# Kernel tuning notes

Hardware: AMD Instinct MI355X
Metric: run time of the kernel (lower is better)

The kernel has to match this reference:

```python
import jax, jax.numpy as jnp
import numpy as np

O = 128      # o_size
E = 512      # embed_dim
H = 128      # h_size
V = 34       # num_letter
B = 2048     # batch
T = 512      # listener timesteps
EPS = 1e-5   # BatchNorm eps


def _lstm_cell(x, h, c, W_ih, W_hh, b_ih, b_hh):
    # PyTorch LSTMCell: gates ordered i, f, g, o
    g = x @ W_ih.T + b_ih + h @ W_hh.T + b_hh
    i, f, gg, o = jnp.split(g, 4, axis=1)
    c_new = jax.nn.sigmoid(f) * c + jax.nn.sigmoid(i) * jnp.tanh(gg)
    h_new = jax.nn.sigmoid(o) * jnp.tanh(c_new)
    return h_new, c_new


def setup_inputs() -> dict:
    key = jax.random.key(0)
    ks = jax.random.split(key, 32)
    d = {}
    d['hk'] = jax.random.normal(ks[0], (B, T, O), jnp.float32)
    d['hv'] = jax.random.normal(ks[1], (B, T, O), jnp.float32)
    d['y_1'] = jax.random.normal(ks[2], (B, E), jnp.float32)
    d['c_1'] = jax.random.normal(ks[3], (B, O), jnp.float32)
    d['sh_1'] = jax.random.normal(ks[4], (3, B, O), jnp.float32)
    d['sc_1'] = jax.random.normal(ks[5], (3, B, O), jnp.float32)
    d['mask'] = jnp.ones((B, T), jnp.float32)
    s = 0.05
    in_dims = [O + E, O, O]
    for l in range(3):
        d[f'W_ih{l}'] = jax.random.normal(ks[6 + 4 * l], (4 * O, in_dims[l]), jnp.float32) * s
        d[f'W_hh{l}'] = jax.random.normal(ks[7 + 4 * l], (4 * O, O), jnp.float32) * s
        d[f'b_ih{l}'] = jax.random.normal(ks[8 + 4 * l], (4 * O,), jnp.float32) * s
        d[f'b_hh{l}'] = jax.random.normal(ks[9 + 4 * l], (4 * O,), jnp.float32) * s
    d['w1'] = jax.random.normal(ks[20], (H, O), jnp.float32) * s
    d['b1'] = jnp.zeros((H,), jnp.float32)
    d['w2'] = jax.random.normal(ks[21], (H, O), jnp.float32) * s
    d['b2'] = jnp.zeros((H,), jnp.float32)
    d['w3'] = jax.random.normal(ks[22], (V, H), jnp.float32) * s
    d['b3'] = jnp.zeros((V,), jnp.float32)
    d['gamma'] = jnp.ones((H,), jnp.float32)
    d['beta'] = jnp.zeros((H,), jnp.float32)
    return d


def reference(hk, hv, y_1, c_1, sh_1, sc_1, mask,
              W_ih0, W_hh0, b_ih0, b_hh0,
              W_ih1, W_hh1, b_ih1, b_hh1,
              W_ih2, W_hh2, b_ih2, b_hh2,
              w1, b1, w2, b2, w3, b3, gamma, beta):
    x0 = jnp.concatenate((y_1, c_1), axis=1)            # [B, E+O]
    sh0, sc0 = _lstm_cell(x0, sh_1[0], sc_1[0], W_ih0, W_hh0, b_ih0, b_hh0)
    sh1, sc1 = _lstm_cell(sh0, sh_1[1], sc_1[1], W_ih1, W_hh1, b_ih1, b_hh1)
    sh2, sc2 = _lstm_cell(sh1, sh_1[2], sc_1[2], W_ih2, W_hh2, b_ih2, b_hh2)

    # Attention: query is the CELL state sc2 (as in the original code)
    scores = jnp.einsum('bto,bo->bt', hk, sc2)           # [B, T]
    p = jax.nn.softmax(scores, axis=1)
    p = p * mask
    p = p / jnp.sum(p, axis=1, keepdims=True)            # mask-then-renormalize
    c = jnp.einsum('bt,bto->bo', p, hv)                  # [B, O]

    out = sh2 @ w1.T + b1 + (c @ w2.T + b2)              # [B, H]
    # BatchNorm1d (training mode: batch statistics, biased variance)
    mu = jnp.mean(out, axis=0)
    var = jnp.mean((out - mu) ** 2, axis=0)
    out = gamma * (out - mu) * jax.lax.rsqrt(var + EPS) + beta
    out = jax.nn.relu(out)
    out = out @ w3.T + b3                                # [B, V]
    out = jax.nn.softmax(out, axis=1)
    return out, c, jnp.stack([sh0, sh1, sh2]), jnp.stack([sc0, sc1, sc2])
```

## Files before the change

### kernel.cpp

```cpp
#include <hip/hip_runtime.h>
#include <hip/hip_bf16.h>

#define BSZ 2048
#define TSZ 512
#define OSZ 128
#define ESZ 512
#define HSZ 128
#define VSZ 34

#define OFF_C   69632
#define OFF_SH  331776
#define OFF_SC  1118208
#define LAYER   262144

typedef __attribute__((ext_vector_type(8))) short s16x8;
typedef __attribute__((ext_vector_type(4))) float f32x4;

__device__ __forceinline__ float sigf(float x)  { return 1.0f / (1.0f + __expf(-x)); }
__device__ __forceinline__ float tanhf_(float x){ return 2.0f / (1.0f + __expf(-2.0f * x)) - 1.0f; }

__device__ __forceinline__ short f2b(float f) {
    return (short)__bfloat16_as_ushort(__float2bfloat16(f));
}

struct F8 { float4 lo, hi; };

__global__ __launch_bounds__(256) void lstm_cell_mfma(
    const float* __restrict__ A0, int w0,
    const float* __restrict__ A1, int w1,
    const float* __restrict__ A2,
    const float* __restrict__ Wih, int in_dim,
    const float* __restrict__ Whh,
    const float* __restrict__ bih, const float* __restrict__ bhh,
    const float* __restrict__ c_prev,
    float* __restrict__ h_out, float* __restrict__ c_out,
    int K)
{
    __shared__ short lsA[64 * 32];
    __shared__ short lsB[64 * 32];

    const int tid = threadIdx.x;
    const int bm = blockIdx.x * 64;
    const int j0 = blockIdx.y * 16;

    const int sRow = tid >> 2;
    const int sKc  = (tid & 3) << 3;
    const int sOff = sRow * 32 + ((((tid & 3)) ^ (sRow & 3)) << 3);

    const int w_row = (sRow >> 4) * 128 + j0 + (sRow & 15);

    const int wav = tid >> 6, lan = tid & 63;
    const int fr  = lan & 15;
    const int fkb = lan >> 4;
    const int aOff = (wav * 16 + fr) * 32 + ((fkb ^ (fr & 3)) << 3);
    const int bOffBase = fr * 32 + ((fkb ^ (fr & 3)) << 3);

    const int j = j0 + fr;

    f32x4 acc[4];
#pragma unroll
    for (int t = 0; t < 4; ++t) {
        float bv = bih[t * 128 + j] + bhh[t * 128 + j];
        acc[t] = (f32x4){bv, bv, bv, bv};
    }

    auto loadA = [&](int kt) -> F8 {
        int kg = kt * 32 + sKc;
        const float* p;
        if (kg < w0)           p = A0 + (size_t)(bm + sRow) * w0 + kg;
        else if (kg < w0 + w1) p = A1 + (size_t)(bm + sRow) * w1 + (kg - w0);
        else                   p = A2 + (size_t)(bm + sRow) * 128 + (kg - w0 - w1);
        F8 r; r.lo = *(const float4*)p; r.hi = *(const float4*)(p + 4); return r;
    };
    auto loadB = [&](int kt) -> F8 {
        int kg = kt * 32 + sKc;
        const float* p;
        if (kg < in_dim) p = Wih + (size_t)w_row * in_dim + kg;
        else             p = Whh + (size_t)w_row * 128 + (kg - in_dim);
        F8 r; r.lo = *(const float4*)p; r.hi = *(const float4*)(p + 4); return r;
    };

    const int nk = K >> 5;
    F8 aV = loadA(0);
    F8 bV = loadB(0);

    for (int kt = 0; kt < nk; ++kt) {
        s16x8 ap, bp;
        ap[0] = f2b(aV.lo.x); ap[1] = f2b(aV.lo.y); ap[2] = f2b(aV.lo.z); ap[3] = f2b(aV.lo.w);
        ap[4] = f2b(aV.hi.x); ap[5] = f2b(aV.hi.y); ap[6] = f2b(aV.hi.z); ap[7] = f2b(aV.hi.w);
        bp[0] = f2b(bV.lo.x); bp[1] = f2b(bV.lo.y); bp[2] = f2b(bV.lo.z); bp[3] = f2b(bV.lo.w);
        bp[4] = f2b(bV.hi.x); bp[5] = f2b(bV.hi.y); bp[6] = f2b(bV.hi.z); bp[7] = f2b(bV.hi.w);
        *(s16x8*)(lsA + sOff) = ap;
        *(s16x8*)(lsB + sOff) = bp;
        __syncthreads();
        if (kt + 1 < nk) { aV = loadA(kt + 1); bV = loadB(kt + 1); }

        s16x8 af = *(const s16x8*)(lsA + aOff);
#pragma unroll
        for (int t = 0; t < 4; ++t) {
            s16x8 bf = *(const s16x8*)(lsB + bOffBase + t * 512);
            acc[t] = __builtin_amdgcn_mfma_f32_16x16x32_bf16(af, bf, acc[t], 0, 0, 0);
        }
        __syncthreads();
    }

#pragma unroll
    for (int r = 0; r < 4; ++r) {
        int row = bm + wav * 16 + fkb * 4 + r;
        float gi = acc[0][r], gf = acc[1][r], gg = acc[2][r], go = acc[3][r];
        float cp = c_prev[(size_t)row * 128 + j];
        float cn = sigf(gf) * cp + sigf(gi) * tanhf_(gg);
        float hn = sigf(go) * tanhf_(cn);
        c_out[(size_t)row * 128 + j] = cn;
        h_out[(size_t)row * 128 + j] = hn;
    }
}

__global__ __launch_bounds__(256) void attn_kernel(
    const float* __restrict__ hk, const float* __restrict__ hv,
    const float* __restrict__ mask, const float* __restrict__ sc2,
    float* __restrict__ c_out)
{
    const int b = blockIdx.x;
    const int tid = threadIdx.x;
    __shared__ float sP[512];
    __shared__ float sRed[8];
    __shared__ float sC[8][128];

    const float* hkb = hk + (size_t)b * (TSZ * OSZ);
    const int og = (tid & 31) * 4;
    const int tg = tid >> 5;
    float4 q = *(const float4*)(sc2 + (size_t)b * 128 + og);

    for (int it = 0; it < 64; ++it) {
        float4 v = *(const float4*)(hkb + it * 1024 + tid * 4);
        float d = v.x * q.x + v.y * q.y + v.z * q.z + v.w * q.w;
        d += __shfl_xor(d, 1, 32);
        d += __shfl_xor(d, 2, 32);
        d += __shfl_xor(d, 4, 32);
        d += __shfl_xor(d, 8, 32);
        d += __shfl_xor(d, 16, 32);
        if ((tid & 31) == 0) sP[it * 8 + tg] = d;
    }
    __syncthreads();

    float m = fmaxf(sP[tid], sP[tid + 256]);
#pragma unroll
    for (int off = 1; off < 64; off <<= 1) m = fmaxf(m, __shfl_xor(m, off, 64));
    if ((tid & 63) == 0) sRed[tid >> 6] = m;
    __syncthreads();
    m = fmaxf(fmaxf(sRed[0], sRed[1]), fmaxf(sRed[2], sRed[3]));

    const float* mk = mask + (size_t)b * TSZ;
    float e0 = __expf(sP[tid] - m) * mk[tid];
    float e1 = __expf(sP[tid + 256] - m) * mk[tid + 256];
    float s = e0 + e1;
#pragma unroll
    for (int off = 1; off < 64; off <<= 1) s += __shfl_xor(s, off, 64);
    if ((tid & 63) == 0) sRed[4 + (tid >> 6)] = s;
    __syncthreads();
    float inv = 1.0f / (sRed[4] + sRed[5] + sRed[6] + sRed[7]);
    sP[tid]       = e0 * inv;
    sP[tid + 256] = e1 * inv;
    __syncthreads();

    float4 acc = {0.f, 0.f, 0.f, 0.f};
    const float* hvb = hv + (size_t)b * (TSZ * OSZ);
    for (int it = 0; it < 64; ++it) {
        float p = sP[it * 8 + tg];
        float4 v = *(const float4*)(hvb + it * 1024 + tid * 4);
        acc.x += p * v.x; acc.y += p * v.y; acc.z += p * v.z; acc.w += p * v.w;
    }
    *(float4*)&sC[tg][og] = acc;
    __syncthreads();
    if (tid < 128) {
        float r = 0.f;
#pragma unroll
        for (int g = 0; g < 8; ++g) r += sC[g][tid];
        c_out[(size_t)b * 128 + tid] = r;
    }
}

__global__ __launch_bounds__(256) void head_pre_kernel(
    const float* __restrict__ sh2, const float* __restrict__ cvec,
    const float* __restrict__ w1, const float* __restrict__ b1,
    const float* __restrict__ w2, const float* __restrict__ b2,
    float* __restrict__ out_pre, float* __restrict__ sum_part,
    float* __restrict__ sq_part)
{
    __shared__ float xs[8][128];
    __shared__ float xc[8][128];
    __shared__ float ps[2][128];
    __shared__ float pq[2][128];
    const int tid = threadIdx.x;
    const int rb = blockIdx.x * 8;
    {
        int row = tid >> 5, off = (tid & 31) * 4;
        *(float4*)&xs[row][off] = *(const float4*)(sh2 + (size_t)(rb + row) * 128 + off);
        *(float4*)&xc[row][off] = *(const float4*)(cvec + (size_t)(rb + row) * 128 + off);
    }
    __syncthreads();

    const int col = tid & 127, rg = tid >> 7;
    float acc[4];
    float bb = b1[col] + b2[col];
#pragma unroll
    for (int r = 0; r < 4; ++r) acc[r] = bb;
    const float* w1r = w1 + (size_t)col * 128;
    const float* w2r = w2 + (size_t)col * 128;
    for (int k4 = 0; k4 < 32; ++k4) {
        float4 wa = *(const float4*)(w1r + k4 * 4);
        float4 wb = *(const float4*)(w2r + k4 * 4);
#pragma unroll
        for (int r = 0; r < 4; ++r) {
            float4 xa = *(const float4*)&xs[rg * 4 + r][k4 * 4];
            float4 xb = *(const float4*)&xc[rg * 4 + r][k4 * 4];
            acc[r] += xa.x * wa.x + xa.y * wa.y + xa.z * wa.z + xa.w * wa.w
                    + xb.x * wb.x + xb.y * wb.y + xb.z * wb.z + xb.w * wb.w;
        }
    }
    float s = 0.f, q = 0.f;
#pragma unroll
    for (int r = 0; r < 4; ++r) {
        out_pre[(size_t)(rb + rg * 4 + r) * 128 + col] = acc[r];
        s += acc[r]; q += acc[r] * acc[r];
    }
    ps[rg][col] = s; pq[rg][col] = q;
    __syncthreads();
    if (rg == 0) {
        sum_part[blockIdx.x * 128 + col] = ps[0][col] + ps[1][col];
        sq_part[blockIdx.x * 128 + col]  = pq[0][col] + pq[1][col];
    }
}

__global__ __launch_bounds__(256) void bn_stats_kernel(
    const float* __restrict__ sum_part, const float* __restrict__ sq_part,
    float* __restrict__ mu_out, float* __restrict__ rstd_out)
{
    __shared__ float s2[2][128], q2[2][128];
    const int tid = threadIdx.x;
    const int col = tid & 127, h = tid >> 7;
    float s = 0.f, q = 0.f;
    for (int p = h * 128; p < h * 128 + 128; ++p) {
        s += sum_part[p * 128 + col];
        q += sq_part[p * 128 + col];
    }
    s2[h][col] = s; q2[h][col] = q;
    __syncthreads();
    if (h == 0) {
        float st = s2[0][col] + s2[1][col];
        float qt = q2[0][col] + q2[1][col];
        float mu = st * (1.0f / 2048.0f);
        float var = qt * (1.0f / 2048.0f) - mu * mu;
        mu_out[col] = mu;
        rstd_out[col] = rsqrtf(var + 1e-5f);
    }
}

__global__ __launch_bounds__(256) void head_post_kernel(
    const float* __restrict__ out_pre, const float* __restrict__ mu_buf,
    const float* __restrict__ rstd_buf, const float* __restrict__ gamma,
    const float* __restrict__ beta, const float* __restrict__ w3,
    const float* __restrict__ b3, float* __restrict__ out0)
{
    __shared__ float xn[8][128];
    __shared__ float lg[8][34];
    const int tid = threadIdx.x;
    const int rb = blockIdx.x * 8;
    {
        int row = tid >> 5, off = (tid & 31) * 4;
        float4 v   = *(const float4*)(out_pre + (size_t)(rb + row) * 128 + off);
        float4 mu4 = *(const float4*)(mu_buf + off);
        float4 rs4 = *(const float4*)(rstd_buf + off);
        float4 g4  = *(const float4*)(gamma + off);
        float4 b4  = *(const float4*)(beta + off);
        float4 o;
        o.x = fmaxf(g4.x * (v.x - mu4.x) * rs4.x + b4.x, 0.0f);
        o.y = fmaxf(g4.y * (v.y - mu4.y) * rs4.y + b4.y, 0.0f);
        o.z = fmaxf(g4.z * (v.z - mu4.z) * rs4.z + b4.z, 0.0f);
        o.w = fmaxf(g4.w * (v.w - mu4.w) * rs4.w + b4.w, 0.0f);
        *(float4*)&xn[row][off] = o;
    }
    __syncthreads();

    for (int idx = tid; idx < 8 * VSZ; idx += 256) {
        int row = idx / VSZ, vv = idx % VSZ;
        const float* w3r = w3 + (size_t)vv * 128;
        float acc = b3[vv];
        for (int k4 = 0; k4 < 32; ++k4) {
            float4 x4 = *(const float4*)&xn[row][k4 * 4];
            float4 wv = *(const float4*)(w3r + k4 * 4);
            acc += x4.x * wv.x + x4.y * wv.y + x4.z * wv.z + x4.w * wv.w;
        }
        lg[row][vv] = acc;
    }
    __syncthreads();

    const int row = tid >> 5, lane = tid & 31;
    float m = -1e30f;
    for (int vv = lane; vv < VSZ; vv += 32) m = fmaxf(m, lg[row][vv]);
#pragma unroll
    for (int off = 1; off < 32; off <<= 1) m = fmaxf(m, __shfl_xor(m, off, 32));
    float e0 = __expf(lg[row][lane] - m);
    float e1 = (lane + 32 < VSZ) ? __expf(lg[row][lane + 32] - m) : 0.0f;
    float s = e0 + e1;
#pragma unroll
    for (int off = 1; off < 32; off <<= 1) s += __shfl_xor(s, off, 32);
    float inv = 1.0f / s;
    out0[(size_t)(rb + row) * VSZ + lane] = e0 * inv;
    if (lane + 32 < VSZ) out0[(size_t)(rb + row) * VSZ + lane + 32] = e1 * inv;
}

extern "C" void kernel_launch(void* const* d_in, const int* in_sizes, int n_in,
                              void* d_out, int out_size, void* d_ws, size_t ws_size,
                              hipStream_t stream)
{
    const float* hk   = (const float*)d_in[0];
    const float* hv   = (const float*)d_in[1];
    const float* y_1  = (const float*)d_in[2];
    const float* c_1  = (const float*)d_in[3];
    const float* sh_1 = (const float*)d_in[4];
    const float* sc_1 = (const float*)d_in[5];
    const float* mask = (const float*)d_in[6];
    const float* Wih0 = (const float*)d_in[7];
    const float* Whh0 = (const float*)d_in[8];
    const float* bih0 = (const float*)d_in[9];
    const float* bhh0 = (const float*)d_in[10];
    const float* Wih1 = (const float*)d_in[11];
    const float* Whh1 = (const float*)d_in[12];
    const float* bih1 = (const float*)d_in[13];
    const float* bhh1 = (const float*)d_in[14];
    const float* Wih2 = (const float*)d_in[15];
    const float* Whh2 = (const float*)d_in[16];
    const float* bih2 = (const float*)d_in[17];
    const float* bhh2 = (const float*)d_in[18];
    const float* w1   = (const float*)d_in[19];
    const float* b1   = (const float*)d_in[20];
    const float* w2   = (const float*)d_in[21];
    const float* b2   = (const float*)d_in[22];
    const float* w3   = (const float*)d_in[23];
    const float* b3   = (const float*)d_in[24];
    const float* gamma= (const float*)d_in[25];
    const float* beta = (const float*)d_in[26];

    float* out   = (float*)d_out;
    float* outC  = out + OFF_C;
    float* outSH = out + OFF_SH;
    float* outSC = out + OFF_SC;

    float* ws       = (float*)d_ws;
    float* out_pre  = ws;
    float* sum_part = ws + 262144;
    float* sq_part  = sum_part + 32768;
    float* mu_buf   = sq_part + 32768;
    float* rstd_buf = mu_buf + 128;

    dim3 gG(32, 8), bG(256);
    lstm_cell_mfma<<<gG, bG, 0, stream>>>(
        y_1, 512, c_1, 128, sh_1, Wih0, 640, Whh0, bih0, bhh0,
        sc_1, outSH, outSC, 768);
    lstm_cell_mfma<<<gG, bG, 0, stream>>>(
        outSH, 128, nullptr, 0, sh_1 + LAYER, Wih1, 128, Whh1, bih1, bhh1,
        sc_1 + LAYER, outSH + LAYER, outSC + LAYER, 256);
    lstm_cell_mfma<<<gG, bG, 0, stream>>>(
        outSH + LAYER, 128, nullptr, 0, sh_1 + 2 * LAYER, Wih2, 128, Whh2, bih2, bhh2,
        sc_1 + 2 * LAYER, outSH + 2 * LAYER, outSC + 2 * LAYER, 256);
    attn_kernel<<<BSZ, 256, 0, stream>>>(hk, hv, mask, outSC + 2 * LAYER, outC);
    head_pre_kernel<<<256, 256, 0, stream>>>(outSH + 2 * LAYER, outC, w1, b1, w2, b2,
                                             out_pre, sum_part, sq_part);
    bn_stats_kernel<<<1, 256, 0, stream>>>(sum_part, sq_part, mu_buf, rstd_buf);
    head_post_kernel<<<256, 256, 0, stream>>>(out_pre, mu_buf, rstd_buf, gamma, beta,
                                              w3, b3, out);
}
```

Baseline: 277.7 us.

## Stage hk through swizzled LDS with register prefetch in attention scores

The score phase now loads 8 timesteps' worth of hk into registers, writes them to a swizzled 32KB shared-memory tile, and prefetches the next chunk while computing dot products. Each thread handles a quarter of a row, so only two shuffles are needed instead of five. The hv loop is also unrolled by 8. The goal is more memory-level parallelism and less shuffle overhead, at the cost of extra LDS use, which may lower occupancy, and extra syncs.

```diff
diff --git a/kernel.cpp b/kernel.cpp
--- a/kernel.cpp
+++ b/kernel.cpp
@@ -123,26 +123,53 @@
 {
     const int b = blockIdx.x;
     const int tid = threadIdx.x;
+    __shared__ float sK[64 * 128];
     __shared__ float sP[512];
     __shared__ float sRed[8];
     __shared__ float sC[8][128];
 
     const float* hkb = hk + (size_t)b * (TSZ * OSZ);
-    const int og = (tid & 31) * 4;
-    const int tg = tid >> 5;
-    float4 q = *(const float4*)(sc2 + (size_t)b * 128 + og);
-
-    for (int it = 0; it < 64; ++it) {
-        float4 v = *(const float4*)(hkb + it * 1024 + tid * 4);
-        float d = v.x * q.x + v.y * q.y + v.z * q.z + v.w * q.w;
-        d += __shfl_xor(d, 1, 32);
-        d += __shfl_xor(d, 2, 32);
-        d += __shfl_xor(d, 4, 32);
-        d += __shfl_xor(d, 8, 32);
-        d += __shfl_xor(d, 16, 32);
-        if ((tid & 31) == 0) sP[it * 8 + tg] = d;
-    }
-    __syncthreads();
+    const float* hvb = hv + (size_t)b * (TSZ * OSZ);
+
+    const int tl = tid >> 2;
+    const int o0 = (tid & 3) << 5;
+    float4 qf[8];
+#pragma unroll
+    for (int k4 = 0; k4 < 8; ++k4)
+        qf[k4] = *(const float4*)(sc2 + (size_t)b * 128 + o0 + k4 * 4);
+
+    const int sT = tid >> 5;
+    const int sO = (tid & 31) << 2;
+
+    float4 pref[8];
+#pragma unroll
+    for (int i = 0; i < 8; ++i)
+        pref[i] = *(const float4*)(hkb + i * 1024 + tid * 4);
+
+    for (int chunk = 0; chunk < 8; ++chunk) {
+#pragma unroll
+        for (int i = 0; i < 8; ++i) {
+            int t = i * 8 + sT;
+            *(float4*)&sK[t * 128 + (sO ^ ((t & 7) << 2))] = pref[i];
+        }
+        __syncthreads();
+        if (chunk < 7) {
+            const float* src = hkb + (chunk + 1) * 8192;
+#pragma unroll
+            for (int i = 0; i < 8; ++i)
+                pref[i] = *(const float4*)(src + i * 1024 + tid * 4);
+        }
+        float d = 0.0f;
+#pragma unroll
+        for (int k4 = 0; k4 < 8; ++k4) {
+            float4 kv = *(const float4*)&sK[tl * 128 + ((o0 + k4 * 4) ^ ((tl & 7) << 2))];
+            d += kv.x * qf[k4].x + kv.y * qf[k4].y + kv.z * qf[k4].z + kv.w * qf[k4].w;
+        }
+        d += __shfl_xor(d, 1, 64);
+        d += __shfl_xor(d, 2, 64);
+        if ((tid & 3) == 0) sP[chunk * 64 + tl] = d;
+        __syncthreads();
+    }
 
     float m = fmaxf(sP[tid], sP[tid + 256]);
 #pragma unroll
@@ -164,8 +191,10 @@
     sP[tid + 256] = e1 * inv;
     __syncthreads();
 
+    const int og = (tid & 31) * 4;
+    const int tg = tid >> 5;
     float4 acc = {0.f, 0.f, 0.f, 0.f};
-    const float* hvb = hv + (size_t)b * (TSZ * OSZ);
+#pragma unroll 8
     for (int it = 0; it < 64; ++it) {
         float p = sP[it * 8 + tg];
         float4 v = *(const float4*)(hvb + it * 1024 + tid * 4);
```

Result: slower. 421.7 us (+51.9%).

## Fuse three LSTM layers into one kernel and fold BN stats into head

Applied to the files above, without the earlier changes.

The three per-layer LSTM cell launches become one kernel. Each 512-thread block owns 16 batch rows across all 512 gate columns and passes h between layers through shared memory instead of global memory. The separate single-block BatchNorm statistics kernel is removed, and every head_post block now reduces the partial sums itself. This saves launches and global round trips, but the LSTM grid shrinks to 128 blocks, each block reloads the full weight matrices, and the BN reduction is repeated in all 256 blocks.

```diff
diff --git a/kernel.cpp b/kernel.cpp
--- a/kernel.cpp
+++ b/kernel.cpp
@@ -25,95 +25,143 @@
 
 struct F8 { float4 lo, hi; };
 
-__global__ __launch_bounds__(256) void lstm_cell_mfma(
-    const float* __restrict__ A0, int w0,
-    const float* __restrict__ A1, int w1,
-    const float* __restrict__ A2,
-    const float* __restrict__ Wih, int in_dim,
-    const float* __restrict__ Whh,
-    const float* __restrict__ bih, const float* __restrict__ bhh,
-    const float* __restrict__ c_prev,
-    float* __restrict__ h_out, float* __restrict__ c_out,
-    int K)
+__global__ __launch_bounds__(512) void lstm_fused_kernel(
+    const float* __restrict__ y_1, const float* __restrict__ c_1,
+    const float* __restrict__ sh_1, const float* __restrict__ sc_1,
+    const float* __restrict__ Wih0, const float* __restrict__ Whh0,
+    const float* __restrict__ bih0, const float* __restrict__ bhh0,
+    const float* __restrict__ Wih1, const float* __restrict__ Whh1,
+    const float* __restrict__ bih1, const float* __restrict__ bhh1,
+    const float* __restrict__ Wih2, const float* __restrict__ Whh2,
+    const float* __restrict__ bih2, const float* __restrict__ bhh2,
+    float* __restrict__ outSH, float* __restrict__ outSC)
 {
-    __shared__ short lsA[64 * 32];
-    __shared__ short lsB[64 * 32];
+    __shared__ short lsA[16 * 32];
+    __shared__ short lsB[512 * 32];
+    __shared__ float hbuf[16 * 128];
 
     const int tid = threadIdx.x;
-    const int bm = blockIdx.x * 64;
-    const int j0 = blockIdx.y * 16;
-
-    const int sRow = tid >> 2;
-    const int sKc  = (tid & 3) << 3;
-    const int sOff = sRow * 32 + ((((tid & 3)) ^ (sRow & 3)) << 3);
-
-    const int w_row = (sRow >> 4) * 128 + j0 + (sRow & 15);
-
-    const int wav = tid >> 6, lan = tid & 63;
-    const int fr  = lan & 15;
-    const int fkb = lan >> 4;
-    const int aOff = (wav * 16 + fr) * 32 + ((fkb ^ (fr & 3)) << 3);
-    const int bOffBase = fr * 32 + ((fkb ^ (fr & 3)) << 3);
-
-    const int j = j0 + fr;
-
-    f32x4 acc[4];
-#pragma unroll
-    for (int t = 0; t < 4; ++t) {
-        float bv = bih[t * 128 + j] + bhh[t * 128 + j];
-        acc[t] = (f32x4){bv, bv, bv, bv};
-    }
-
-    auto loadA = [&](int kt) -> F8 {
-        int kg = kt * 32 + sKc;
-        const float* p;
-        if (kg < w0)           p = A0 + (size_t)(bm + sRow) * w0 + kg;
-        else if (kg < w0 + w1) p = A1 + (size_t)(bm + sRow) * w1 + (kg - w0);
-        else                   p = A2 + (size_t)(bm + sRow) * 128 + (kg - w0 - w1);
-        F8 r; r.lo = *(const float4*)p; r.hi = *(const float4*)(p + 4); return r;
+    const int bm = blockIdx.x * 16;
+
+    const int sRowA = (tid >> 2) & 15;
+    const int sKcA  = (tid & 3) << 3;
+    const int aStOff = sRowA * 32 + (((tid & 3) ^ (sRowA & 3)) << 3);
+
+    const int sRowB = tid >> 2;
+    const int bSwz  = (((tid & 3) ^ (sRowB & 3)) << 3);
+    int wRow[4];
+#pragma unroll
+    for (int i = 0; i < 4; ++i) {
+        int nn = sRowB + i * 128;
+        wRow[i] = ((nn >> 4) & 3) * 128 + ((nn >> 6) << 4) + (nn & 15);
+    }
+
+    const int wv = tid >> 6, lan = tid & 63;
+    const int fr = lan & 15, fkb = lan >> 4;
+    const int aOff = fr * 32 + ((fkb ^ (fr & 3)) << 3);
+    const int bOffBase = (wv * 64 + fr) * 32 + ((fkb ^ (fr & 3)) << 3);
+    const int j = wv * 16 + fr;
+
+    auto run_cell = [&](int mode,
+                        const float* A0, int w0, const float* A1, int w1,
+                        const float* A2,
+                        const float* Wih, int in_dim, const float* Whh,
+                        const float* bih, const float* bhh,
+                        const float* cprev_g,
+                        float* hout_g, float* cout_g,
+                        bool writeHbuf, int K)
+    {
+        f32x4 acc[4];
+#pragma unroll
+        for (int a = 0; a < 4; ++a) {
+            float bv = bih[a * 128 + j] + bhh[a * 128 + j];
+            acc[a] = (f32x4){bv, bv, bv, bv};
+        }
+
+        auto loadA = [&](int kt) -> F8 {
+            int kg = kt * 32 + sKcA;
+            F8 r;
+            if (mode == 0) {
+                const float* p;
+                if (kg < w0)           p = A0 + (size_t)(bm + sRowA) * w0 + kg;
+                else if (kg < w0 + w1) p = A1 + (size_t)(bm + sRowA) * w1 + (kg - w0);
+                else                   p = A2 + (size_t)(bm + sRowA) * 128 + (kg - w0 - w1);
+                r.lo = *(const float4*)p; r.hi = *(const float4*)(p + 4);
+            } else {
+                if (kg < 128) {
+                    const float* p = &hbuf[sRowA * 128 + kg];
+                    r.lo = *(const float4*)p; r.hi = *(const float4*)(p + 4);
+                } else {
+                    const float* p = A2 + (size_t)(bm + sRowA) * 128 + (kg - 128);
+                    r.lo = *(const float4*)p; r.hi = *(const float4*)(p + 4);
+                }
+            }
+            return r;
+        };
+        auto loadB = [&](int kt, int i) -> F8 {
+            int kg = kt * 32 + ((tid & 3) << 3);
+            const float* p;
+            if (kg < in_dim) p = Wih + (size_t)wRow[i] * in_dim + kg;
+            else             p = Whh + (size_t)wRow[i] * 128 + (kg - in_dim);
+            F8 r; r.lo = *(const float4*)p; r.hi = *(const float4*)(p + 4); return r;
+        };
+
+        const int nk = K >> 5;
+        F8 aV; F8 bV[4];
+        if (tid < 64) aV = loadA(0);
+#pragma unroll
+        for (int i = 0; i < 4; ++i) bV[i] = loadB(0, i);
+
+        for (int kt = 0; kt < nk; ++kt) {
+            if (tid < 64) {
+                s16x8 ap;
+                ap[0] = f2b(aV.lo.x); ap[1] = f2b(aV.lo.y); ap[2] = f2b(aV.lo.z); ap[3] = f2b(aV.lo.w);
+                ap[4] = f2b(aV.hi.x); ap[5] = f2b(aV.hi.y); ap[6] = f2b(aV.hi.z); ap[7] = f2b(aV.hi.w);
+                *(s16x8*)(lsA + aStOff) = ap;
+            }
+#pragma unroll
+            for (int i = 0; i < 4; ++i) {
+                s16x8 bp;
+                bp[0] = f2b(bV[i].lo.x); bp[1] = f2b(bV[i].lo.y); bp[2] = f2b(bV[i].lo.z); bp[3] = f2b(bV[i].lo.w);
+                bp[4] = f2b(bV[i].hi.x); bp[5] = f2b(bV[i].hi.y); bp[6] = f2b(bV[i].hi.z); bp[7] = f2b(bV[i].hi.w);
+                *(s16x8*)(lsB + (sRowB + i * 128) * 32 + bSwz) = bp;
+            }
+            __syncthreads();
+            if (kt + 1 < nk) {
+                if (tid < 64) aV = loadA(kt + 1);
+#pragma unroll
+                for (int i = 0; i < 4; ++i) bV[i] = loadB(kt + 1, i);
+            }
+            s16x8 af = *(const s16x8*)(lsA + aOff);
+#pragma unroll
+            for (int a = 0; a < 4; ++a) {
+                s16x8 bf = *(const s16x8*)(lsB + bOffBase + a * 512);
+                acc[a] = __builtin_amdgcn_mfma_f32_16x16x32_bf16(af, bf, acc[a], 0, 0, 0);
+            }
+            __syncthreads();
+        }
+
+#pragma unroll
+        for (int r = 0; r < 4; ++r) {
+            int row_l = fkb * 4 + r;
+            int row = bm + row_l;
+            float gi = acc[0][r], gf = acc[1][r], gg = acc[2][r], go = acc[3][r];
+            float cp = cprev_g[(size_t)row * 128 + j];
+            float cn = sigf(gf) * cp + sigf(gi) * tanhf_(gg);
+            float hn = sigf(go) * tanhf_(cn);
+            cout_g[(size_t)row * 128 + j] = cn;
+            hout_g[(size_t)row * 128 + j] = hn;
+            if (writeHbuf) hbuf[row_l * 128 + j] = hn;
+        }
+        __syncthreads();
     };
-    auto loadB = [&](int kt) -> F8 {
-        int kg = kt * 32 + sKc;
-        const float* p;
-        if (kg < in_dim) p = Wih + (size_t)w_row * in_dim + kg;
-        else             p = Whh + (size_t)w_row * 128 + (kg - in_dim);
-        F8 r; r.lo = *(const float4*)p; r.hi = *(const float4*)(p + 4); return r;
-    };
-
-    const int nk = K >> 5;
-    F8 aV = loadA(0);
-    F8 bV = loadB(0);
-
-    for (int kt = 0; kt < nk; ++kt) {
-        s16x8 ap, bp;
-        ap[0] = f2b(aV.lo.x); ap[1] = f2b(aV.lo.y); ap[2] = f2b(aV.lo.z); ap[3] = f2b(aV.lo.w);
-        ap[4] = f2b(aV.hi.x); ap[5] = f2b(aV.hi.y); ap[6] = f2b(aV.hi.z); ap[7] = f2b(aV.hi.w);
-        bp[0] = f2b(bV.lo.x); bp[1] = f2b(bV.lo.y); bp[2] = f2b(bV.lo.z); bp[3] = f2b(bV.lo.w);
-        bp[4] = f2b(bV.hi.x); bp[5] = f2b(bV.hi.y); bp[6] = f2b(bV.hi.z); bp[7] = f2b(bV.hi.w);
-        *(s16x8*)(lsA + sOff) = ap;
-        *(s16x8*)(lsB + sOff) = bp;
-        __syncthreads();
-        if (kt + 1 < nk) { aV = loadA(kt + 1); bV = loadB(kt + 1); }
-
-        s16x8 af = *(const s16x8*)(lsA + aOff);
-#pragma unroll
-        for (int t = 0; t < 4; ++t) {
-            s16x8 bf = *(const s16x8*)(lsB + bOffBase + t * 512);
-            acc[t] = __builtin_amdgcn_mfma_f32_16x16x32_bf16(af, bf, acc[t], 0, 0, 0);
-        }
-        __syncthreads();
-    }
-
-#pragma unroll
-    for (int r = 0; r < 4; ++r) {
-        int row = bm + wav * 16 + fkb * 4 + r;
-        float gi = acc[0][r], gf = acc[1][r], gg = acc[2][r], go = acc[3][r];
-        float cp = c_prev[(size_t)row * 128 + j];
-        float cn = sigf(gf) * cp + sigf(gi) * tanhf_(gg);
-        float hn = sigf(go) * tanhf_(cn);
-        c_out[(size_t)row * 128 + j] = cn;
-        h_out[(size_t)row * 128 + j] = hn;
-    }
+
+    run_cell(0, y_1, 512, c_1, 128, sh_1, Wih0, 640, Whh0, bih0, bhh0,
+             sc_1, outSH, outSC, true, 768);
+    run_cell(1, nullptr, 0, nullptr, 0, sh_1 + LAYER, Wih1, 128, Whh1, bih1, bhh1,
+             sc_1 + LAYER, outSH + LAYER, outSC + LAYER, true, 256);
+    run_cell(1, nullptr, 0, nullptr, 0, sh_1 + 2 * LAYER, Wih2, 128, Whh2, bih2, bhh2,
+             sc_1 + 2 * LAYER, outSH + 2 * LAYER, outSC + 2 * LAYER, false, 256);
 }
 
 __global__ __launch_bounds__(256) void attn_kernel(
@@ -233,45 +281,44 @@
     }
 }
 
-__global__ __launch_bounds__(256) void bn_stats_kernel(
-    const float* __restrict__ sum_part, const float* __restrict__ sq_part,
-    float* __restrict__ mu_out, float* __restrict__ rstd_out)
-{
-    __shared__ float s2[2][128], q2[2][128];
-    const int tid = threadIdx.x;
-    const int col = tid & 127, h = tid >> 7;
-    float s = 0.f, q = 0.f;
-    for (int p = h * 128; p < h * 128 + 128; ++p) {
-        s += sum_part[p * 128 + col];
-        q += sq_part[p * 128 + col];
-    }
-    s2[h][col] = s; q2[h][col] = q;
-    __syncthreads();
-    if (h == 0) {
-        float st = s2[0][col] + s2[1][col];
-        float qt = q2[0][col] + q2[1][col];
-        float mu = st * (1.0f / 2048.0f);
-        float var = qt * (1.0f / 2048.0f) - mu * mu;
-        mu_out[col] = mu;
-        rstd_out[col] = rsqrtf(var + 1e-5f);
-    }
-}
-
 __global__ __launch_bounds__(256) void head_post_kernel(
-    const float* __restrict__ out_pre, const float* __restrict__ mu_buf,
-    const float* __restrict__ rstd_buf, const float* __restrict__ gamma,
+    const float* __restrict__ out_pre, const float* __restrict__ sum_part,
+    const float* __restrict__ sq_part, const float* __restrict__ gamma,
     const float* __restrict__ beta, const float* __restrict__ w3,
     const float* __restrict__ b3, float* __restrict__ out0)
 {
+    __shared__ float s2[2][128], q2[2][128];
+    __shared__ float sMu[128], sRs[128];
     __shared__ float xn[8][128];
     __shared__ float lg[8][34];
     const int tid = threadIdx.x;
     const int rb = blockIdx.x * 8;
+
+    {
+        const int col = tid & 127, h = tid >> 7;
+        float s = 0.f, q = 0.f;
+        for (int p = h * 128; p < h * 128 + 128; ++p) {
+            s += sum_part[p * 128 + col];
+            q += sq_part[p * 128 + col];
+        }
+        s2[h][col] = s; q2[h][col] = q;
+        __syncthreads();
+        if (h == 0) {
+            float st = s2[0][col] + s2[1][col];
+            float qt = q2[0][col] + q2[1][col];
+            float mu = st * (1.0f / 2048.0f);
+            float var = qt * (1.0f / 2048.0f) - mu * mu;
+            sMu[col] = mu;
+            sRs[col] = rsqrtf(var + 1e-5f);
+        }
+        __syncthreads();
+    }
+
     {
         int row = tid >> 5, off = (tid & 31) * 4;
         float4 v   = *(const float4*)(out_pre + (size_t)(rb + row) * 128 + off);
-        float4 mu4 = *(const float4*)(mu_buf + off);
-        float4 rs4 = *(const float4*)(rstd_buf + off);
+        float4 mu4 = *(const float4*)&sMu[off];
+        float4 rs4 = *(const float4*)&sRs[off];
         float4 g4  = *(const float4*)(gamma + off);
         float4 b4  = *(const float4*)(beta + off);
         float4 o;
@@ -352,23 +399,16 @@
     float* out_pre  = ws;
     float* sum_part = ws + 262144;
     float* sq_part  = sum_part + 32768;
-    float* mu_buf   = sq_part + 32768;
-    float* rstd_buf = mu_buf + 128;
-
-    dim3 gG(32, 8), bG(256);
-    lstm_cell_mfma<<<gG, bG, 0, stream>>>(
-        y_1, 512, c_1, 128, sh_1, Wih0, 640, Whh0, bih0, bhh0,
-        sc_1, outSH, outSC, 768);
-    lstm_cell_mfma<<<gG, bG, 0, stream>>>(
-        outSH, 128, nullptr, 0, sh_1 + LAYER, Wih1, 128, Whh1, bih1, bhh1,
-        sc_1 + LAYER, outSH + LAYER, outSC + LAYER, 256);
-    lstm_cell_mfma<<<gG, bG, 0, stream>>>(
-        outSH + LAYER, 128, nullptr, 0, sh_1 + 2 * LAYER, Wih2, 128, Whh2, bih2, bhh2,
-        sc_1 + 2 * LAYER, outSH + 2 * LAYER, outSC + 2 * LAYER, 256);
+
+    lstm_fused_kernel<<<128, 512, 0, stream>>>(
+        y_1, c_1, sh_1, sc_1,
+        Wih0, Whh0, bih0, bhh0,
+        Wih1, Whh1, bih1, bhh1,
+        Wih2, Whh2, bih2, bhh2,
+        outSH, outSC);
     attn_kernel<<<BSZ, 256, 0, stream>>>(hk, hv, mask, outSC + 2 * LAYER, outC);
     head_pre_kernel<<<256, 256, 0, stream>>>(outSH + 2 * LAYER, outC, w1, b1, w2, b2,
                                              out_pre, sum_part, sq_part);
-    bn_stats_kernel<<<1, 256, 0, stream>>>(sum_part, sq_part, mu_buf, rstd_buf);
-    head_post_kernel<<<256, 256, 0, stream>>>(out_pre, mu_buf, rstd_buf, gamma, beta,
+    head_post_kernel<<<256, 256, 0, stream>>>(out_pre, sum_part, sq_part, gamma, beta,
                                               w3, b3, out);
 }
```

After: 306.6 us. +10.4%, slower.

## Merge LSTM layers and head kernels into cooperative launches with grid sync

Applied to the files above, without the earlier changes.

The three per-layer LSTM launches become one cooperative kernel that separates layers with grid-wide syncs. The head_pre, bn_stats and head_post kernels become a second cooperative kernel in which every block redundantly reduces the BatchNorm partials after a grid sync. This removes several kernel launches and their inter-kernel gaps. In exchange it adds grid barrier cost, repeats the partial-sum reduction in all 256 blocks, and needs every block to be co-resident.

```diff
diff --git a/kernel.cpp b/kernel.cpp
--- a/kernel.cpp
+++ b/kernel.cpp
@@ -1,5 +1,8 @@
 #include <hip/hip_runtime.h>
 #include <hip/hip_bf16.h>
+#include <hip/hip_cooperative_groups.h>
+
+namespace cg = cooperative_groups;
 
 #define BSZ 2048
 #define TSZ 512
@@ -25,7 +28,7 @@
 
 struct F8 { float4 lo, hi; };
 
-__global__ __launch_bounds__(256) void lstm_cell_mfma(
+__device__ void lstm_cell_body(
     const float* __restrict__ A0, int w0,
     const float* __restrict__ A1, int w1,
     const float* __restrict__ A2,
@@ -34,11 +37,8 @@
     const float* __restrict__ bih, const float* __restrict__ bhh,
     const float* __restrict__ c_prev,
     float* __restrict__ h_out, float* __restrict__ c_out,
-    int K)
+    int K, short* lsA, short* lsB)
 {
-    __shared__ short lsA[64 * 32];
-    __shared__ short lsB[64 * 32];
-
     const int tid = threadIdx.x;
     const int bm = blockIdx.x * 64;
     const int j0 = blockIdx.y * 16;
@@ -116,6 +116,35 @@
     }
 }
 
+__global__ __launch_bounds__(256) void lstm_coop_kernel(
+    const float* __restrict__ y_1, const float* __restrict__ c_1,
+    const float* __restrict__ sh_1, const float* __restrict__ sc_1,
+    const float* __restrict__ Wih0, const float* __restrict__ Whh0,
+    const float* __restrict__ bih0, const float* __restrict__ bhh0,
+    const float* __restrict__ Wih1, const float* __restrict__ Whh1,
+    const float* __restrict__ bih1, const float* __restrict__ bhh1,
+    const float* __restrict__ Wih2, const float* __restrict__ Whh2,
+    const float* __restrict__ bih2, const float* __restrict__ bhh2,
+    float* __restrict__ outSH, float* __restrict__ outSC)
+{
+    __shared__ short lsA[64 * 32];
+    __shared__ short lsB[64 * 32];
+    cg::grid_group grid = cg::this_grid();
+
+    lstm_cell_body(y_1, 512, c_1, 128, sh_1, Wih0, 640, Whh0, bih0, bhh0,
+                   sc_1, outSH, outSC, 768, lsA, lsB);
+    __threadfence();
+    grid.sync();
+    lstm_cell_body(outSH, 128, nullptr, 0, sh_1 + LAYER, Wih1, 128, Whh1,
+                   bih1, bhh1, sc_1 + LAYER, outSH + LAYER, outSC + LAYER,
+                   256, lsA, lsB);
+    __threadfence();
+    grid.sync();
+    lstm_cell_body(outSH + LAYER, 128, nullptr, 0, sh_1 + 2 * LAYER, Wih2, 128,
+                   Whh2, bih2, bhh2, sc_1 + 2 * LAYER, outSH + 2 * LAYER,
+                   outSC + 2 * LAYER, 256, lsA, lsB);
+}
+
 __global__ __launch_bounds__(256) void attn_kernel(
     const float* __restrict__ hk, const float* __restrict__ hv,
     const float* __restrict__ mask, const float* __restrict__ sc2,
@@ -181,19 +210,26 @@
     }
 }
 
-__global__ __launch_bounds__(256) void head_pre_kernel(
+__global__ __launch_bounds__(256) void head_coop_kernel(
     const float* __restrict__ sh2, const float* __restrict__ cvec,
     const float* __restrict__ w1, const float* __restrict__ b1,
     const float* __restrict__ w2, const float* __restrict__ b2,
     float* __restrict__ out_pre, float* __restrict__ sum_part,
-    float* __restrict__ sq_part)
+    float* __restrict__ sq_part, const float* __restrict__ gamma,
+    const float* __restrict__ beta, const float* __restrict__ w3,
+    const float* __restrict__ b3, float* __restrict__ out0)
 {
     __shared__ float xs[8][128];
     __shared__ float xc[8][128];
     __shared__ float ps[2][128];
     __shared__ float pq[2][128];
+    __shared__ float sMu[128], sRs[128];
+    __shared__ float lg[8][34];
+
+    cg::grid_group gridg = cg::this_grid();
     const int tid = threadIdx.x;
     const int rb = blockIdx.x * 8;
+
     {
         int row = tid >> 5, off = (tid & 31) * 4;
         *(float4*)&xs[row][off] = *(const float4*)(sh2 + (size_t)(rb + row) * 128 + off);
@@ -202,76 +238,64 @@
     __syncthreads();
 
     const int col = tid & 127, rg = tid >> 7;
-    float acc[4];
-    float bb = b1[col] + b2[col];
-#pragma unroll
-    for (int r = 0; r < 4; ++r) acc[r] = bb;
-    const float* w1r = w1 + (size_t)col * 128;
-    const float* w2r = w2 + (size_t)col * 128;
-    for (int k4 = 0; k4 < 32; ++k4) {
-        float4 wa = *(const float4*)(w1r + k4 * 4);
-        float4 wb = *(const float4*)(w2r + k4 * 4);
+    {
+        float acc[4];
+        float bb = b1[col] + b2[col];
+#pragma unroll
+        for (int r = 0; r < 4; ++r) acc[r] = bb;
+        const float* w1r = w1 + (size_t)col * 128;
+        const float* w2r = w2 + (size_t)col * 128;
+        for (int k4 = 0; k4 < 32; ++k4) {
+            float4 wa = *(const float4*)(w1r + k4 * 4);
+            float4 wb = *(const float4*)(w2r + k4 * 4);
+#pragma unroll
+            for (int r = 0; r < 4; ++r) {
+                float4 xa = *(const float4*)&xs[rg * 4 + r][k4 * 4];
+                float4 xb = *(const float4*)&xc[rg * 4 + r][k4 * 4];
+                acc[r] += xa.x * wa.x + xa.y * wa.y + xa.z * wa.z + xa.w * wa.w
+                        + xb.x * wb.x + xb.y * wb.y + xb.z * wb.z + xb.w * wb.w;
+            }
+        }
+        float s = 0.f, q = 0.f;
 #pragma unroll
         for (int r = 0; r < 4; ++r) {
-            float4 xa = *(const float4*)&xs[rg * 4 + r][k4 * 4];
-            float4 xb = *(const float4*)&xc[rg * 4 + r][k4 * 4];
-            acc[r] += xa.x * wa.x + xa.y * wa.y + xa.z * wa.z + xa.w * wa.w
-                    + xb.x * wb.x + xb.y * wb.y + xb.z * wb.z + xb.w * wb.w;
-        }
-    }
-    float s = 0.f, q = 0.f;
-#pragma unroll
-    for (int r = 0; r < 4; ++r) {
-        out_pre[(size_t)(rb + rg * 4 + r) * 128 + col] = acc[r];
-        s += acc[r]; q += acc[r] * acc[r];
-    }
-    ps[rg][col] = s; pq[rg][col] = q;
-    __syncthreads();
-    if (rg == 0) {
-        sum_part[blockIdx.x * 128 + col] = ps[0][col] + ps[1][col];
-        sq_part[blockIdx.x * 128 + col]  = pq[0][col] + pq[1][col];
-    }
-}
-
-__global__ __launch_bounds__(256) void bn_stats_kernel(
-    const float* __restrict__ sum_part, const float* __restrict__ sq_part,
-    float* __restrict__ mu_out, float* __restrict__ rstd_out)
-{
-    __shared__ float s2[2][128], q2[2][128];
-    const int tid = threadIdx.x;
-    const int col = tid & 127, h = tid >> 7;
-    float s = 0.f, q = 0.f;
-    for (int p = h * 128; p < h * 128 + 128; ++p) {
-        s += sum_part[p * 128 + col];
-        q += sq_part[p * 128 + col];
-    }
-    s2[h][col] = s; q2[h][col] = q;
-    __syncthreads();
-    if (h == 0) {
-        float st = s2[0][col] + s2[1][col];
-        float qt = q2[0][col] + q2[1][col];
-        float mu = st * (1.0f / 2048.0f);
-        float var = qt * (1.0f / 2048.0f) - mu * mu;
-        mu_out[col] = mu;
-        rstd_out[col] = rsqrtf(var + 1e-5f);
-    }
-}
-
-__global__ __launch_bounds__(256) void head_post_kernel(
-    const float* __restrict__ out_pre, const float* __restrict__ mu_buf,
-    const float* __restrict__ rstd_buf, const float* __restrict__ gamma,
-    const float* __restrict__ beta, const float* __restrict__ w3,
-    const float* __restrict__ b3, float* __restrict__ out0)
-{
-    __shared__ float xn[8][128];
-    __shared__ float lg[8][34];
-    const int tid = threadIdx.x;
-    const int rb = blockIdx.x * 8;
+            out_pre[(size_t)(rb + rg * 4 + r) * 128 + col] = acc[r];
+            s += acc[r]; q += acc[r] * acc[r];
+        }
+        ps[rg][col] = s; pq[rg][col] = q;
+        __syncthreads();
+        if (rg == 0) {
+            sum_part[blockIdx.x * 128 + col] = ps[0][col] + ps[1][col];
+            sq_part[blockIdx.x * 128 + col]  = pq[0][col] + pq[1][col];
+        }
+    }
+    __threadfence();
+    gridg.sync();
+
+    {
+        float s = 0.f, q = 0.f;
+        for (int p = rg * 128; p < rg * 128 + 128; ++p) {
+            s += sum_part[p * 128 + col];
+            q += sq_part[p * 128 + col];
+        }
+        ps[rg][col] = s; pq[rg][col] = q;
+        __syncthreads();
+        if (rg == 0) {
+            float st = ps[0][col] + ps[1][col];
+            float qt = pq[0][col] + pq[1][col];
+            float mu = st * (1.0f / 2048.0f);
+            float var = qt * (1.0f / 2048.0f) - mu * mu;
+            sMu[col] = mu;
+            sRs[col] = rsqrtf(var + 1e-5f);
+        }
+        __syncthreads();
+    }
+
     {
         int row = tid >> 5, off = (tid & 31) * 4;
         float4 v   = *(const float4*)(out_pre + (size_t)(rb + row) * 128 + off);
-        float4 mu4 = *(const float4*)(mu_buf + off);
-        float4 rs4 = *(const float4*)(rstd_buf + off);
+        float4 mu4 = *(const float4*)&sMu[off];
+        float4 rs4 = *(const float4*)&sRs[off];
         float4 g4  = *(const float4*)(gamma + off);
         float4 b4  = *(const float4*)(beta + off);
         float4 o;
@@ -279,7 +303,7 @@
         o.y = fmaxf(g4.y * (v.y - mu4.y) * rs4.y + b4.y, 0.0f);
         o.z = fmaxf(g4.z * (v.z - mu4.z) * rs4.z + b4.z, 0.0f);
         o.w = fmaxf(g4.w * (v.w - mu4.w) * rs4.w + b4.w, 0.0f);
-        *(float4*)&xn[row][off] = o;
+        *(float4*)&xs[row][off] = o;
     }
     __syncthreads();
 
@@ -288,7 +312,7 @@
         const float* w3r = w3 + (size_t)vv * 128;
         float acc = b3[vv];
         for (int k4 = 0; k4 < 32; ++k4) {
-            float4 x4 = *(const float4*)&xn[row][k4 * 4];
+            float4 x4 = *(const float4*)&xs[row][k4 * 4];
             float4 wv = *(const float4*)(w3r + k4 * 4);
             acc += x4.x * wv.x + x4.y * wv.y + x4.z * wv.z + x4.w * wv.w;
         }
@@ -352,23 +376,28 @@
     float* out_pre  = ws;
     float* sum_part = ws + 262144;
     float* sq_part  = sum_part + 32768;
-    float* mu_buf   = sq_part + 32768;
-    float* rstd_buf = mu_buf + 128;
-
-    dim3 gG(32, 8), bG(256);
-    lstm_cell_mfma<<<gG, bG, 0, stream>>>(
-        y_1, 512, c_1, 128, sh_1, Wih0, 640, Whh0, bih0, bhh0,
-        sc_1, outSH, outSC, 768);
-    lstm_cell_mfma<<<gG, bG, 0, stream>>>(
-        outSH, 128, nullptr, 0, sh_1 + LAYER, Wih1, 128, Whh1, bih1, bhh1,
-        sc_1 + LAYER, outSH + LAYER, outSC + LAYER, 256);
-    lstm_cell_mfma<<<gG, bG, 0, stream>>>(
-        outSH + LAYER, 128, nullptr, 0, sh_1 + 2 * LAYER, Wih2, 128, Whh2, bih2, bhh2,
-        sc_1 + 2 * LAYER, outSH + 2 * LAYER, outSC + 2 * LAYER, 256);
+
+    {
+        void* args[] = {
+            (void*)&y_1, (void*)&c_1, (void*)&sh_1, (void*)&sc_1,
+            (void*)&Wih0, (void*)&Whh0, (void*)&bih0, (void*)&bhh0,
+            (void*)&Wih1, (void*)&Whh1, (void*)&bih1, (void*)&bhh1,
+            (void*)&Wih2, (void*)&Whh2, (void*)&bih2, (void*)&bhh2,
+            (void*)&outSH, (void*)&outSC
+        };
+        hipLaunchCooperativeKernel((void*)lstm_coop_kernel, dim3(32, 8),
+                                   dim3(256), args, 0, stream);
+    }
     attn_kernel<<<BSZ, 256, 0, stream>>>(hk, hv, mask, outSC + 2 * LAYER, outC);
-    head_pre_kernel<<<256, 256, 0, stream>>>(outSH + 2 * LAYER, outC, w1, b1, w2, b2,
-                                             out_pre, sum_part, sq_part);
-    bn_stats_kernel<<<1, 256, 0, stream>>>(sum_part, sq_part, mu_buf, rstd_buf);
-    head_post_kernel<<<256, 256, 0, stream>>>(out_pre, mu_buf, rstd_buf, gamma, beta,
-                                              w3, b3, out);
-}
+    {
+        const float* sh2 = outSH + 2 * LAYER;
+        void* args[] = {
+            (void*)&sh2, (void*)&outC, (void*)&w1, (void*)&b1,
+            (void*)&w2, (void*)&b2, (void*)&out_pre, (void*)&sum_part,
+            (void*)&sq_part, (void*)&gamma, (void*)&beta, (void*)&w3,
+            (void*)&b3, (void*)&out
+        };
+        hipLaunchCooperativeKernel((void*)head_coop_kernel, dim3(256),
+                                   dim3(256), args, 0, stream);
+    }
+}
```

New measurement: 429.4 us. 1.55x slower.
